# Kernel optimization log

Measured on AMD Instinct MI355X. Metric: run time of the kernel, lower is better.

The kernel has to match this reference:

```python
import jax, jax.numpy as jnp
import numpy as np

DIM = 2048
N_HEADS = 16
N_KV_HEADS = 4
HEAD_DIM = DIM // N_HEADS  # 128
N_REP = N_HEADS // N_KV_HEADS  # 4
B, S = 8, 1024
ROPE_THETA = 10000.0


def _rope_tables(seq_len, head_dim, theta=ROPE_THETA):
    inv_freq = 1.0 / (theta ** (np.arange(0, head_dim, 2, dtype=np.float32) / head_dim))
    t = np.arange(seq_len, dtype=np.float32)
    freqs = np.outer(t, inv_freq)  # [S, head_dim//2]
    return jnp.asarray(np.cos(freqs)), jnp.asarray(np.sin(freqs))


def setup_inputs() -> dict:
    key = jax.random.key(0)
    ks = jax.random.split(key, 5)
    x = jax.random.normal(ks[0], (B, S, DIM), dtype=jnp.float32)
    wq = jax.random.normal(ks[1], (N_HEADS * HEAD_DIM, DIM), dtype=jnp.float32) * (DIM ** -0.5)
    wk = jax.random.normal(ks[2], (N_KV_HEADS * HEAD_DIM, DIM), dtype=jnp.float32) * (DIM ** -0.5)
    wv = jax.random.normal(ks[3], (N_KV_HEADS * HEAD_DIM, DIM), dtype=jnp.float32) * (DIM ** -0.5)
    wo = jax.random.normal(ks[4], (N_HEADS * HEAD_DIM, DIM), dtype=jnp.float32).T * (DIM ** -0.5)
    freqs_cos, freqs_sin = _rope_tables(S, HEAD_DIM)
    return {"x": x, "freqs_cos": freqs_cos, "freqs_sin": freqs_sin,
            "wq": wq, "wk": wk, "wv": wv, "wo": wo}


def _apply_rope(t, cos, sin):
    # t: [B, S, H, head_dim]; cos/sin: [S, head_dim//2]
    t2 = t.reshape(*t.shape[:-1], HEAD_DIM // 2, 2)
    tr, ti = t2[..., 0], t2[..., 1]
    c = cos[None, :, None, :]
    s = sin[None, :, None, :]
    out_r = tr * c - ti * s
    out_i = tr * s + ti * c
    return jnp.stack([out_r, out_i], axis=-1).reshape(t.shape)


def reference(x, freqs_cos, freqs_sin, wq, wk, wv, wo):
    b, s, _ = x.shape
    xq = (x @ wq.T).reshape(b, s, N_HEADS, HEAD_DIM)
    xk = (x @ wk.T).reshape(b, s, N_KV_HEADS, HEAD_DIM)
    xv = (x @ wv.T).reshape(b, s, N_KV_HEADS, HEAD_DIM)

    xq = _apply_rope(xq, freqs_cos, freqs_sin)
    xk = _apply_rope(xk, freqs_cos, freqs_sin)

    # GQA without materializing repeat_interleave: group heads [B,S,G,R,hd]
    xq = xq.reshape(b, s, N_KV_HEADS, N_REP, HEAD_DIM)
    scale = 1.0 / jnp.sqrt(jnp.float32(HEAD_DIM))
    scores = jnp.einsum('bqgrd,bkgd->bgrqk', xq, xk) * scale  # [B,G,R,S,S]

    causal = jnp.tril(jnp.ones((s, s), dtype=bool))
    scores = jnp.where(causal, scores, jnp.finfo(scores.dtype).min)
    probs = jax.nn.softmax(scores, axis=-1)

    out = jnp.einsum('bgrqk,bkgd->bqgrd', probs, xv)  # [B,S,G,R,hd]
    out = out.reshape(b, s, N_HEADS * HEAD_DIM)
    return out @ wo.T
```

## Files before the change

kernel.cpp:

```cpp
#include <hip/hip_runtime.h>

typedef unsigned short u16;
typedef unsigned int   u32;
typedef short v8s __attribute__((ext_vector_type(8)));
typedef float v4f __attribute__((ext_vector_type(4)));

#define DIMM 2048
#define NH   16
#define NKV  4
#define HD   128
#define BB   8
#define SS   1024
#define KVD  (NKV*HD)
#define KSCL 0.12751744f
#define THR  11.5f
#define EXP2(x) __builtin_amdgcn_exp2f(x)

__device__ __forceinline__ u16 f2b(float f) {
  u32 u = __builtin_bit_cast(u32, f);
  u32 r = (u + 0x7FFFu + ((u >> 16) & 1u)) >> 16;
  return (u16)r;
}
__device__ __forceinline__ float b2f(u16 h) {
  return __builtin_bit_cast(float, (u32)h << 16);
}

typedef const u32 __attribute__((address_space(1)))* gp_t;
typedef u32 __attribute__((address_space(3)))* lp_t;
__device__ __forceinline__ void async16(const u16* g, u16* l) {
  __builtin_amdgcn_global_load_lds((gp_t)g, (lp_t)l, 16, 0, 0);
}

__global__ __launch_bounds__(256) void convert_all(
    const float* __restrict__ x, const float* __restrict__ wq,
    const float* __restrict__ wk, const float* __restrict__ wv,
    const float* __restrict__ wo,
    u16* __restrict__ xb, u16* __restrict__ wqb, u16* __restrict__ wkb,
    u16* __restrict__ wvb, u16* __restrict__ wob) {
  u32 t = blockIdx.x * 256u + threadIdx.x;
  const float* src; u16* dst; u32 lc;
  if      (t < 2097152u) { src = x;  dst = xb;  lc = t; }
  else if (t < 2621440u) { src = wq; dst = wqb; lc = t - 2097152u; }
  else if (t < 2752512u) { src = wk; dst = wkb; lc = t - 2621440u; }
  else if (t < 2883584u) { src = wv; dst = wvb; lc = t - 2752512u; }
  else                   { src = wo; dst = wob; lc = t - 2883584u; }
  size_t e = (size_t)lc * 8;
  float4 a = *(const float4*)(src + e);
  float4 b = *(const float4*)(src + e + 4);
  uint4 o;
  o.x = (u32)f2b(a.x) | ((u32)f2b(a.y) << 16);
  o.y = (u32)f2b(a.z) | ((u32)f2b(a.w) << 16);
  o.z = (u32)f2b(b.x) | ((u32)f2b(b.y) << 16);
  o.w = (u32)f2b(b.z) | ((u32)f2b(b.w) << 16);
  *(uint4*)(dst + e) = o;
}

template<int OUTF>
__global__ __launch_bounds__(256) void gemm_bt(
    const u16* __restrict__ A, const u16* __restrict__ Bw,
    float* __restrict__ Cf, u16* __restrict__ Cb, int M, int N, int K) {
  __shared__ u16 As[4096];
  __shared__ u16 Bs[4096];
  int wave = threadIdx.x >> 6, lane = threadIdx.x & 63;
  int lo = lane & 15, hi = lane >> 4;
  int wm = wave >> 1, wn = wave & 1;
  int m0 = blockIdx.y * 128, n0 = blockIdx.x * 128;
  v4f acc[4][4] = {};
  for (int k0 = 0; k0 < K; k0 += 32) {
    __syncthreads();
#pragma unroll
    for (int j = 0; j < 2; ++j) {
      int base = (j * 4 + wave) * 512;
      int l = base + lane * 8;
      int row = l >> 5, col = l & 31;
      async16(A  + (size_t)(m0 + row) * K + k0 + col, &As[base]);
      async16(Bw + (size_t)(n0 + row) * K + k0 + col, &Bs[base]);
    }
    __syncthreads();
    v8s af[4], bf[4];
#pragma unroll
    for (int t = 0; t < 4; ++t) {
      af[t] = *(const v8s*)&As[(wm * 64 + t * 16 + lo) * 32 + hi * 8];
      bf[t] = *(const v8s*)&Bs[(wn * 64 + t * 16 + lo) * 32 + hi * 8];
    }
#pragma unroll
    for (int mt = 0; mt < 4; ++mt)
#pragma unroll
      for (int nt = 0; nt < 4; ++nt)
        acc[mt][nt] = __builtin_amdgcn_mfma_f32_16x16x32_bf16(af[mt], bf[nt], acc[mt][nt], 0, 0, 0);
  }
#pragma unroll
  for (int mt = 0; mt < 4; ++mt)
#pragma unroll
    for (int nt = 0; nt < 4; ++nt)
#pragma unroll
      for (int r = 0; r < 4; ++r) {
        int row = m0 + wm * 64 + mt * 16 + 4 * hi + r;
        int col = n0 + wn * 64 + nt * 16 + lo;
        if (OUTF) Cf[(size_t)row * N + col] = acc[mt][nt][r];
        else      Cb[(size_t)row * N + col] = f2b(acc[mt][nt][r]);
      }
}

__global__ __launch_bounds__(256) void rope_all(
    u16* __restrict__ Qb, u16* __restrict__ Kb,
    const float* __restrict__ fc, const float* __restrict__ fs) {
  u32 t = blockIdx.x * 256u + threadIdx.x;
  u16* buf; u32 row, c8, stride; float sc;
  if (t < 2097152u) { buf = Qb; row = t >> 8; c8 = (t & 255u) * 8u; stride = 2048u; sc = 1.0f; }
  else { u32 lc = t - 2097152u; buf = Kb; row = lc >> 6; c8 = (lc & 63u) * 8u; stride = 512u; sc = KSCL; }
  u32 sp = row & 1023u;
  u32 j0 = (c8 & 127u) >> 1;
  float4 c = *(const float4*)(fc + (size_t)sp * 64 + j0);
  float4 s = *(const float4*)(fs + (size_t)sp * 64 + j0);
  u16* p = buf + (size_t)row * stride + c8;
  uint4 w = *(const uint4*)p;
  u32 wv_[4] = {w.x, w.y, w.z, w.w};
  float cc[4] = {c.x, c.y, c.z, c.w};
  float ss2[4] = {s.x, s.y, s.z, s.w};
#pragma unroll
  for (int i = 0; i < 4; ++i) {
    float tr = b2f((u16)(wv_[i] & 0xFFFFu));
    float ti = b2f((u16)(wv_[i] >> 16));
    float orr = (tr * cc[i] - ti * ss2[i]) * sc;
    float oi  = (tr * ss2[i] + ti * cc[i]) * sc;
    wv_[i] = (u32)f2b(orr) | ((u32)f2b(oi) << 16);
  }
  uint4 o; o.x = wv_[0]; o.y = wv_[1]; o.z = wv_[2]; o.w = wv_[3];
  *(uint4*)p = o;
}

__global__ __launch_bounds__(256) void transpose_v(
    const u16* __restrict__ vb, u16* __restrict__ vt) {
  __shared__ u32 t32[64][33];
  int blk = blockIdx.x;
  int dt = blk & 1, st = (blk >> 1) & 15, kvh = (blk >> 5) & 3, b = blk >> 7;
  int s0 = st * 64, d0 = dt * 64;
  int tid = threadIdx.x;
  int r = tid >> 3, q = tid & 7;
  const u16* src = vb + (size_t)b * SS * KVD + (size_t)kvh * HD + d0;
#pragma unroll
  for (int p = 0; p < 2; ++p) {
    int row = p * 32 + r;
    uint4 v = *(const uint4*)(src + (size_t)(s0 + row) * KVD + q * 8);
    t32[row][q * 4 + 0] = v.x; t32[row][q * 4 + 1] = v.y;
    t32[row][q * 4 + 2] = v.z; t32[row][q * 4 + 3] = v.w;
  }
  __syncthreads();
  const u16* t16 = (const u16*)t32;
  u16* dst = vt + ((size_t)(b * NKV + kvh) * HD + d0) * SS + s0;
#pragma unroll
  for (int p = 0; p < 2; ++p) {
    int dd = p * 32 + r;
    u16 tmp[8];
#pragma unroll
    for (int j = 0; j < 8; ++j) tmp[j] = t16[(size_t)(q * 8 + j) * 66 + dd];
    *(uint4*)(dst + (size_t)dd * SS + q * 8) = *(uint4*)tmp;
  }
}

__global__ __launch_bounds__(512, 4) void attn(
    const u16* __restrict__ Q, const u16* __restrict__ Kb,
    const u16* __restrict__ Vt, u16* __restrict__ AO) {
  __shared__ u16 Ksh[2][8192];
  __shared__ u16 Vsh[2][8192];
  __shared__ u16 plds[8][1024];
  int blk = blockIdx.x;
  int qc2 = blk & 7;
  int h   = (blk >> 3) & 15;
  int b   = blk >> 7;
  int wave = threadIdx.x >> 6;
  int lane = threadIdx.x & 63;
  int lo = lane & 15, hi = lane >> 4;
  int q0 = qc2 * 128 + wave * 16;
  int kvh = h >> 2;
  const u16* Qp = Q  + (size_t)b * SS * DIMM + (size_t)h * HD;
  const u16* Kp = Kb + (size_t)b * SS * KVD + (size_t)kvh * HD;
  const u16* Vp = Vt + (size_t)(b * NKV + kvh) * HD * SS;

  int l4 = lane >> 4, l4s = lane & 15;
  int l8 = lane >> 3, l8s = lane & 7;

  v8s qf[4];
#pragma unroll
  for (int ks = 0; ks < 4; ++ks)
    qf[ks] = *(const v8s*)(Qp + (size_t)(q0 + lo) * DIMM + ks * 32 + hi * 8);

  float M[4], Lp[4];
  v4f oacc[8];
#pragma unroll
  for (int r = 0; r < 4; ++r) { M[r] = -1e30f; Lp[r] = 0.f; }
#pragma unroll
  for (int nt = 0; nt < 8; ++nt) oacc[nt] = (v4f){0.f, 0.f, 0.f, 0.f};

  int NT = 2 * qc2 + 2;

#pragma unroll
  for (int i = 0; i < 2; ++i) {
    int instr = wave * 2 + i;
    int row = instr * 4 + l4;
    async16(Kp + (size_t)row * KVD + ((l4s ^ (row & 7)) * 8), &Ksh[0][instr * 512]);
    int d = instr * 8 + l8;
    async16(Vp + (size_t)d * SS + ((l8s ^ (d & 7)) * 8), &Vsh[0][instr * 512]);
  }
  asm volatile("s_waitcnt vmcnt(0)" ::: "memory");
  __builtin_amdgcn_s_barrier();
  __builtin_amdgcn_sched_barrier(0);

  int cur = 0;
  for (int t = 0; t < NT; ++t) {
    int kv0 = t * 64;
    if (t + 1 < NT) {
      int kv1 = kv0 + 64;
#pragma unroll
      for (int i = 0; i < 2; ++i) {
        int instr = wave * 2 + i;
        int row = instr * 4 + l4;
        async16(Kp + (size_t)(kv1 + row) * KVD + ((l4s ^ (row & 7)) * 8),
                &Ksh[cur ^ 1][instr * 512]);
        int d = instr * 8 + l8;
        async16(Vp + (size_t)d * SS + kv1 + ((l8s ^ (d & 7)) * 8),
                &Vsh[cur ^ 1][instr * 512]);
      }
    }
    if (kv0 <= q0 + 15) {
      const u16* Kbuf = Ksh[cur];
      const u16* Vbuf = Vsh[cur];
      v4f sacc[4] = {(v4f){0,0,0,0},(v4f){0,0,0,0},(v4f){0,0,0,0},(v4f){0,0,0,0}};
      __builtin_amdgcn_s_setprio(1);
#pragma unroll
      for (int ks = 0; ks < 4; ++ks)
#pragma unroll
        for (int tt = 0; tt < 4; ++tt) {
          int krow = tt * 16 + lo;
          v8s kf = *(const v8s*)&Kbuf[krow * 128 + (((ks * 4 + hi) ^ (krow & 7)) * 8)];
          sacc[tt] = __builtin_amdgcn_mfma_f32_16x16x32_bf16(qf[ks], kf, sacc[tt], 0, 0, 0);
        }
      __builtin_amdgcn_s_setprio(0);
      bool masked = (kv0 + 63 > q0);
      float s_[4][4], pmax[4];
#pragma unroll
      for (int r = 0; r < 4; ++r) {
        int qg = q0 + 4 * hi + r;
#pragma unroll
        for (int tt = 0; tt < 4; ++tt) {
          s_[r][tt] = sacc[tt][r];
          if (masked && (kv0 + tt * 16 + lo > qg)) s_[r][tt] = -1e30f;
        }
        pmax[r] = fmaxf(fmaxf(s_[r][0], s_[r][1]), fmaxf(s_[r][2], s_[r][3]));
      }
      bool need = (pmax[0] > M[0] + THR) || (pmax[1] > M[1] + THR) ||
                  (pmax[2] > M[2] + THR) || (pmax[3] > M[3] + THR);
      if (__any(need)) {
#pragma unroll
        for (int r = 0; r < 4; ++r) {
          float mx = pmax[r];
          mx = fmaxf(mx, __shfl_xor(mx, 1));
          mx = fmaxf(mx, __shfl_xor(mx, 2));
          mx = fmaxf(mx, __shfl_xor(mx, 4));
          mx = fmaxf(mx, __shfl_xor(mx, 8));
          float mnew = fmaxf(M[r], mx);
          float a = EXP2(M[r] - mnew);
          M[r] = mnew; Lp[r] *= a;
#pragma unroll
          for (int nt = 0; nt < 8; ++nt) oacc[nt][r] *= a;
        }
      }
#pragma unroll
      for (int r = 0; r < 4; ++r) {
        int row = 4 * hi + r;
#pragma unroll
        for (int tt = 0; tt < 4; ++tt) {
          float p = EXP2(s_[r][tt] - M[r]);
          Lp[r] += p;
          plds[wave][row * 64 + (((tt * 16) + lo) ^ ((row & 7) << 3))] = f2b(p);
        }
      }
      v8s pf0 = *(const v8s*)&plds[wave][lo * 64 + ((hi ^ (lo & 7)) * 8)];
      v8s pf1 = *(const v8s*)&plds[wave][lo * 64 + (((4 + hi) ^ (lo & 7)) * 8)];
      __builtin_amdgcn_s_setprio(1);
#pragma unroll
      for (int nt = 0; nt < 8; ++nt) {
        int vd = nt * 16 + lo;
        v8s vf0 = *(const v8s*)&Vbuf[vd * 64 + ((hi ^ (vd & 7)) * 8)];
        oacc[nt] = __builtin_amdgcn_mfma_f32_16x16x32_bf16(pf0, vf0, oacc[nt], 0, 0, 0);
        v8s vf1 = *(const v8s*)&Vbuf[vd * 64 + (((4 + hi) ^ (vd & 7)) * 8)];
        oacc[nt] = __builtin_amdgcn_mfma_f32_16x16x32_bf16(pf1, vf1, oacc[nt], 0, 0, 0);
      }
      __builtin_amdgcn_s_setprio(0);
    }
    asm volatile("s_waitcnt vmcnt(0)" ::: "memory");
    __builtin_amdgcn_s_barrier();
    __builtin_amdgcn_sched_barrier(0);
    cur ^= 1;
  }
  float L[4];
#pragma unroll
  for (int r = 0; r < 4; ++r) {
    float l = Lp[r];
    l += __shfl_xor(l, 1);
    l += __shfl_xor(l, 2);
    l += __shfl_xor(l, 4);
    l += __shfl_xor(l, 8);
    L[r] = l;
  }
  u16* Op = AO + (size_t)b * SS * DIMM + (size_t)h * HD;
#pragma unroll
  for (int nt = 0; nt < 8; ++nt)
#pragma unroll
    for (int r = 0; r < 4; ++r)
      Op[(size_t)(q0 + 4 * hi + r) * DIMM + nt * 16 + lo] = f2b(oacc[nt][r] / L[r]);
}

extern "C" void kernel_launch(void* const* d_in, const int* in_sizes, int n_in,
                              void* d_out, int out_size, void* d_ws, size_t ws_size,
                              hipStream_t stream) {
  const float* x  = (const float*)d_in[0];
  const float* fc = (const float*)d_in[1];
  const float* fs = (const float*)d_in[2];
  const float* wq = (const float*)d_in[3];
  const float* wk = (const float*)d_in[4];
  const float* wv = (const float*)d_in[5];
  const float* wo = (const float*)d_in[6];
  float* out = (float*)d_out;

  u16* ws  = (u16*)d_ws;
  u16* xb  = ws;
  u16* wqb = xb  + 16777216;
  u16* wkb = wqb + 4194304;
  u16* wvb = wkb + 1048576;
  u16* wob = wvb + 1048576;
  u16* qb  = wob + 4194304;
  u16* kb  = qb  + 16777216;
  u16* vb  = kb  + 4194304;
  u16* ao  = vb  + 4194304;
  u16* vtb = wqb;

  convert_all<<<13312, 256, 0, stream>>>(x, wq, wk, wv, wo, xb, wqb, wkb, wvb, wob);
  gemm_bt<0><<<dim3(16, 64), 256, 0, stream>>>(xb, wqb, nullptr, qb, 8192, 2048, 2048);
  gemm_bt<0><<<dim3(4, 64),  256, 0, stream>>>(xb, wkb, nullptr, kb, 8192, 512, 2048);
  gemm_bt<0><<<dim3(4, 64),  256, 0, stream>>>(xb, wvb, nullptr, vb, 8192, 512, 2048);
  rope_all<<<10240, 256, 0, stream>>>(qb, kb, fc, fs);
  transpose_v<<<1024, 256, 0, stream>>>(vb, vtb);
  attn<<<1024, 512, 0, stream>>>(qb, kb, vtb, ao);
  gemm_bt<1><<<dim3(16, 64), 256, 0, stream>>>(ao, wob, out, nullptr, 8192, 2048, 2048);
}
```

Baseline: 578.5 us.

## Fuse QKV projections into one GEMM and use pipelined 256x128 tiles

The separate Q, K and V projection GEMMs are merged into a single GEMM against a concatenated weight matrix, writing one interleaved QKV buffer that rope, transpose and attention read with a new stride. The GEMM kernel moves to 512 threads with 256x128 output tiles, a BK of 64, double-buffered async LDS loads with an XOR swizzle, a grouped block-index swizzle for L2 locality, and raised MFMA priority. This is meant to cut launch count, improve operand reuse and hide global-load latency. In exchange it uses more LDS and registers per block, and the QKV GEMM no longer divides evenly into waves across the CUs.

```diff
diff --git a/kernel.cpp b/kernel.cpp
--- a/kernel.cpp
+++ b/kernel.cpp
@@ -11,7 +11,7 @@
 #define HD   128
 #define BB   8
 #define SS   1024
-#define KVD  (NKV*HD)
+#define QKVD 3072
 #define KSCL 0.12751744f
 #define THR  11.5f
 #define EXP2(x) __builtin_amdgcn_exp2f(x)
@@ -56,64 +56,105 @@
 }
 
 template<int OUTF>
-__global__ __launch_bounds__(256) void gemm_bt(
+__global__ __launch_bounds__(512, 2) void gemm256(
     const u16* __restrict__ A, const u16* __restrict__ Bw,
-    float* __restrict__ Cf, u16* __restrict__ Cb, int M, int N, int K) {
-  __shared__ u16 As[4096];
-  __shared__ u16 Bs[4096];
-  int wave = threadIdx.x >> 6, lane = threadIdx.x & 63;
+    float* __restrict__ Cf, u16* __restrict__ Cb, int M, int N, int K, int NX) {
+  __shared__ u16 Ash[2][256 * 64];
+  __shared__ u16 Bsh[2][128 * 64];
+  int tid = threadIdx.x;
+  int wave = tid >> 6, lane = tid & 63;
   int lo = lane & 15, hi = lane >> 4;
-  int wm = wave >> 1, wn = wave & 1;
-  int m0 = blockIdx.y * 128, n0 = blockIdx.x * 128;
+  int wr = wave >> 1, wc = wave & 1;
+  int nwg = gridDim.x;
+  int id = blockIdx.x;
+  int swz = (id & 7) * (nwg >> 3) + (id >> 3);
+  int bx = swz % NX, by = swz / NX;
+  int m0 = by * 256, n0 = bx * 128;
+  int NK = K >> 6;
+
+#define STAGE_G(buf, kt)                                                      \
+  {                                                                           \
+    _Pragma("unroll")                                                         \
+    for (int i = 0; i < 4; ++i) {                                             \
+      int s = i * 512 + tid;                                                  \
+      int row = s >> 3, c = s & 7;                                            \
+      async16(A + (size_t)(m0 + row) * K + (kt) * 64 + ((c ^ (row & 7)) * 8), \
+              &Ash[buf][s * 8]);                                              \
+    }                                                                         \
+    _Pragma("unroll")                                                         \
+    for (int i = 0; i < 2; ++i) {                                             \
+      int s = i * 512 + tid;                                                  \
+      int row = s >> 3, c = s & 7;                                            \
+      async16(Bw + (size_t)(n0 + row) * K + (kt) * 64 + ((c ^ (row & 7)) * 8),\
+              &Bsh[buf][s * 8]);                                              \
+    }                                                                         \
+  }
+
   v4f acc[4][4] = {};
-  for (int k0 = 0; k0 < K; k0 += 32) {
-    __syncthreads();
-#pragma unroll
-    for (int j = 0; j < 2; ++j) {
-      int base = (j * 4 + wave) * 512;
-      int l = base + lane * 8;
-      int row = l >> 5, col = l & 31;
-      async16(A  + (size_t)(m0 + row) * K + k0 + col, &As[base]);
-      async16(Bw + (size_t)(n0 + row) * K + k0 + col, &Bs[base]);
+  STAGE_G(0, 0);
+  STAGE_G(1, 1);
+  int cur = 0;
+  for (int kt = 0; kt < NK; ++kt) {
+    if (kt + 1 < NK) asm volatile("s_waitcnt vmcnt(6)" ::: "memory");
+    else             asm volatile("s_waitcnt vmcnt(0)" ::: "memory");
+    __builtin_amdgcn_s_barrier();
+    const u16* Ab = Ash[cur];
+    const u16* Bb = Bsh[cur];
+#pragma unroll
+    for (int ks2 = 0; ks2 < 2; ++ks2) {
+      v8s af[4], bf[4];
+#pragma unroll
+      for (int mf = 0; mf < 4; ++mf) {
+        int row = wr * 64 + mf * 16 + lo;
+        af[mf] = *(const v8s*)&Ab[row * 64 + (((ks2 * 4 + hi) ^ (row & 7)) * 8)];
+      }
+#pragma unroll
+      for (int nf = 0; nf < 4; ++nf) {
+        int row = wc * 64 + nf * 16 + lo;
+        bf[nf] = *(const v8s*)&Bb[row * 64 + (((ks2 * 4 + hi) ^ (row & 7)) * 8)];
+      }
+      if (ks2 == 1) {
+        asm volatile("s_waitcnt lgkmcnt(0)" ::: "memory");
+        __builtin_amdgcn_s_barrier();
+        if (kt + 2 < NK) STAGE_G(cur, kt + 2);
+      }
+      __builtin_amdgcn_s_setprio(1);
+#pragma unroll
+      for (int mf = 0; mf < 4; ++mf)
+#pragma unroll
+        for (int nf = 0; nf < 4; ++nf)
+          acc[mf][nf] = __builtin_amdgcn_mfma_f32_16x16x32_bf16(af[mf], bf[nf], acc[mf][nf], 0, 0, 0);
+      __builtin_amdgcn_s_setprio(0);
     }
-    __syncthreads();
-    v8s af[4], bf[4];
-#pragma unroll
-    for (int t = 0; t < 4; ++t) {
-      af[t] = *(const v8s*)&As[(wm * 64 + t * 16 + lo) * 32 + hi * 8];
-      bf[t] = *(const v8s*)&Bs[(wn * 64 + t * 16 + lo) * 32 + hi * 8];
-    }
-#pragma unroll
-    for (int mt = 0; mt < 4; ++mt)
-#pragma unroll
-      for (int nt = 0; nt < 4; ++nt)
-        acc[mt][nt] = __builtin_amdgcn_mfma_f32_16x16x32_bf16(af[mt], bf[nt], acc[mt][nt], 0, 0, 0);
-  }
-#pragma unroll
-  for (int mt = 0; mt < 4; ++mt)
-#pragma unroll
-    for (int nt = 0; nt < 4; ++nt)
+    cur ^= 1;
+  }
+#pragma unroll
+  for (int mf = 0; mf < 4; ++mf)
+#pragma unroll
+    for (int nf = 0; nf < 4; ++nf)
 #pragma unroll
       for (int r = 0; r < 4; ++r) {
-        int row = m0 + wm * 64 + mt * 16 + 4 * hi + r;
-        int col = n0 + wn * 64 + nt * 16 + lo;
-        if (OUTF) Cf[(size_t)row * N + col] = acc[mt][nt][r];
-        else      Cb[(size_t)row * N + col] = f2b(acc[mt][nt][r]);
-      }
+        int row = m0 + wr * 64 + mf * 16 + 4 * hi + r;
+        int col = n0 + wc * 64 + nf * 16 + lo;
+        if (OUTF) Cf[(size_t)row * N + col] = acc[mf][nf][r];
+        else      Cb[(size_t)row * N + col] = f2b(acc[mf][nf][r]);
+      }
+#undef STAGE_G
 }
 
 __global__ __launch_bounds__(256) void rope_all(
-    u16* __restrict__ Qb, u16* __restrict__ Kb,
+    u16* __restrict__ qkv,
     const float* __restrict__ fc, const float* __restrict__ fs) {
   u32 t = blockIdx.x * 256u + threadIdx.x;
-  u16* buf; u32 row, c8, stride; float sc;
-  if (t < 2097152u) { buf = Qb; row = t >> 8; c8 = (t & 255u) * 8u; stride = 2048u; sc = 1.0f; }
-  else { u32 lc = t - 2097152u; buf = Kb; row = lc >> 6; c8 = (lc & 63u) * 8u; stride = 512u; sc = KSCL; }
+  u16* p; u32 row, c8; float sc;
+  if (t < 2097152u) { row = t >> 8; c8 = (t & 255u) * 8u;
+                      p = qkv + (size_t)row * QKVD + c8; sc = 1.0f; }
+  else { u32 lc = t - 2097152u; row = lc >> 6; c8 = (lc & 63u) * 8u;
+         p = qkv + (size_t)row * QKVD + 2048 + c8; sc = KSCL; }
   u32 sp = row & 1023u;
   u32 j0 = (c8 & 127u) >> 1;
   float4 c = *(const float4*)(fc + (size_t)sp * 64 + j0);
   float4 s = *(const float4*)(fs + (size_t)sp * 64 + j0);
-  u16* p = buf + (size_t)row * stride + c8;
   uint4 w = *(const uint4*)p;
   u32 wv_[4] = {w.x, w.y, w.z, w.w};
   float cc[4] = {c.x, c.y, c.z, c.w};
@@ -131,18 +172,18 @@
 }
 
 __global__ __launch_bounds__(256) void transpose_v(
-    const u16* __restrict__ vb, u16* __restrict__ vt) {
+    const u16* __restrict__ qkv, u16* __restrict__ vt) {
   __shared__ u32 t32[64][33];
   int blk = blockIdx.x;
   int dt = blk & 1, st = (blk >> 1) & 15, kvh = (blk >> 5) & 3, b = blk >> 7;
   int s0 = st * 64, d0 = dt * 64;
   int tid = threadIdx.x;
   int r = tid >> 3, q = tid & 7;
-  const u16* src = vb + (size_t)b * SS * KVD + (size_t)kvh * HD + d0;
+  const u16* src = qkv + (size_t)b * SS * QKVD + 2560 + kvh * HD + d0;
 #pragma unroll
   for (int p = 0; p < 2; ++p) {
     int row = p * 32 + r;
-    uint4 v = *(const uint4*)(src + (size_t)(s0 + row) * KVD + q * 8);
+    uint4 v = *(const uint4*)(src + (size_t)(s0 + row) * QKVD + q * 8);
     t32[row][q * 4 + 0] = v.x; t32[row][q * 4 + 1] = v.y;
     t32[row][q * 4 + 2] = v.z; t32[row][q * 4 + 3] = v.w;
   }
@@ -160,8 +201,8 @@
 }
 
 __global__ __launch_bounds__(512, 4) void attn(
-    const u16* __restrict__ Q, const u16* __restrict__ Kb,
-    const u16* __restrict__ Vt, u16* __restrict__ AO) {
+    const u16* __restrict__ qkv, const u16* __restrict__ Vt,
+    u16* __restrict__ AO) {
   __shared__ u16 Ksh[2][8192];
   __shared__ u16 Vsh[2][8192];
   __shared__ u16 plds[8][1024];
@@ -174,8 +215,8 @@
   int lo = lane & 15, hi = lane >> 4;
   int q0 = qc2 * 128 + wave * 16;
   int kvh = h >> 2;
-  const u16* Qp = Q  + (size_t)b * SS * DIMM + (size_t)h * HD;
-  const u16* Kp = Kb + (size_t)b * SS * KVD + (size_t)kvh * HD;
+  const u16* Qp = qkv + (size_t)b * SS * QKVD + h * HD;
+  const u16* Kp = qkv + (size_t)b * SS * QKVD + 2048 + kvh * HD;
   const u16* Vp = Vt + (size_t)(b * NKV + kvh) * HD * SS;
 
   int l4 = lane >> 4, l4s = lane & 15;
@@ -184,7 +225,7 @@
   v8s qf[4];
 #pragma unroll
   for (int ks = 0; ks < 4; ++ks)
-    qf[ks] = *(const v8s*)(Qp + (size_t)(q0 + lo) * DIMM + ks * 32 + hi * 8);
+    qf[ks] = *(const v8s*)(Qp + (size_t)(q0 + lo) * QKVD + ks * 32 + hi * 8);
 
   float M[4], Lp[4];
   v4f oacc[8];
@@ -199,7 +240,7 @@
   for (int i = 0; i < 2; ++i) {
     int instr = wave * 2 + i;
     int row = instr * 4 + l4;
-    async16(Kp + (size_t)row * KVD + ((l4s ^ (row & 7)) * 8), &Ksh[0][instr * 512]);
+    async16(Kp + (size_t)row * QKVD + ((l4s ^ (row & 7)) * 8), &Ksh[0][instr * 512]);
     int d = instr * 8 + l8;
     async16(Vp + (size_t)d * SS + ((l8s ^ (d & 7)) * 8), &Vsh[0][instr * 512]);
   }
@@ -216,7 +257,7 @@
       for (int i = 0; i < 2; ++i) {
         int instr = wave * 2 + i;
         int row = instr * 4 + l4;
-        async16(Kp + (size_t)(kv1 + row) * KVD + ((l4s ^ (row & 7)) * 8),
+        async16(Kp + (size_t)(kv1 + row) * QKVD + ((l4s ^ (row & 7)) * 8),
                 &Ksh[cur ^ 1][instr * 512]);
         int d = instr * 8 + l8;
         async16(Vp + (size_t)d * SS + kv1 + ((l8s ^ (d & 7)) * 8),
@@ -304,7 +345,7 @@
     l += __shfl_xor(l, 8);
     L[r] = l;
   }
-  u16* Op = AO + (size_t)b * SS * DIMM + (size_t)h * HD;
+  u16* Op = AO + (size_t)b * SS * DIMM + h * HD;
 #pragma unroll
   for (int nt = 0; nt < 8; ++nt)
 #pragma unroll
@@ -324,24 +365,19 @@
   const float* wo = (const float*)d_in[6];
   float* out = (float*)d_out;
 
-  u16* ws  = (u16*)d_ws;
-  u16* xb  = ws;
-  u16* wqb = xb  + 16777216;
-  u16* wkb = wqb + 4194304;
-  u16* wvb = wkb + 1048576;
-  u16* wob = wvb + 1048576;
-  u16* qb  = wob + 4194304;
-  u16* kb  = qb  + 16777216;
-  u16* vb  = kb  + 4194304;
-  u16* ao  = vb  + 4194304;
-  u16* vtb = wqb;
-
-  convert_all<<<13312, 256, 0, stream>>>(x, wq, wk, wv, wo, xb, wqb, wkb, wvb, wob);
-  gemm_bt<0><<<dim3(16, 64), 256, 0, stream>>>(xb, wqb, nullptr, qb, 8192, 2048, 2048);
-  gemm_bt<0><<<dim3(4, 64),  256, 0, stream>>>(xb, wkb, nullptr, kb, 8192, 512, 2048);
-  gemm_bt<0><<<dim3(4, 64),  256, 0, stream>>>(xb, wvb, nullptr, vb, 8192, 512, 2048);
-  rope_all<<<10240, 256, 0, stream>>>(qb, kb, fc, fs);
-  transpose_v<<<1024, 256, 0, stream>>>(vb, vtb);
-  attn<<<1024, 512, 0, stream>>>(qb, kb, vtb, ao);
-  gemm_bt<1><<<dim3(16, 64), 256, 0, stream>>>(ao, wob, out, nullptr, 8192, 2048, 2048);
-}
+  u16* ws   = (u16*)d_ws;
+  u16* xb   = ws;
+  u16* wqkv = xb + 16777216;
+  u16* wob  = wqkv + 6291456;
+  u16* qkvb = wob + 4194304;
+  u16* ao   = qkvb + 25165824;
+  u16* vtb  = wqkv;
+
+  convert_all<<<13312, 256, 0, stream>>>(x, wq, wk, wv, wo, xb,
+      wqkv, wqkv + 4194304, wqkv + 5242880, wob);
+  gemm256<0><<<768, 512, 0, stream>>>(xb, wqkv, nullptr, qkvb, 8192, 3072, 2048, 24);
+  rope_all<<<10240, 256, 0, stream>>>(qkvb, fc, fs);
+  transpose_v<<<1024, 256, 0, stream>>>(qkvb, vtb);
+  attn<<<1024, 512, 0, stream>>>(qkvb, vtb, ao);
+  gemm256<1><<<512, 512, 0, stream>>>(ao, wob, out, nullptr, 8192, 2048, 2048, 16);
+}
```

New measurement: 481.0 us. -16.9%, faster.
